# Performance work log

Measured on AMD Instinct MI355X. Metric: run time of the kernel, lower is better.

Reference implementation:

```python
import jax, jax.numpy as jnp
import numpy as np

N = 2_097_152  # number of pose pairs


def _skew(w):
    # w: [N,3] -> [N,3,3] skew-symmetric matrices
    x, y, z = w[..., 0], w[..., 1], w[..., 2]
    O = jnp.zeros_like(x)
    return jnp.stack([
        jnp.stack([O, -z, y], -1),
        jnp.stack([z, O, -x], -1),
        jnp.stack([-y, x, O], -1),
    ], -2)


def _exp_se3(xi):
    # xi: [N,6] twist = [rot_vec(3), trans(3)] -> (R:[N,3,3], t:[N,3])
    w, v = xi[..., :3], xi[..., 3:]
    t2 = jnp.sum(w * w, -1)                      # theta^2
    small = t2 < 1e-8
    t2s = jnp.where(small, 1.0, t2)              # safe denominator
    th = jnp.sqrt(t2s)
    A = jnp.where(small, 1.0 - t2 / 6.0, jnp.sin(th) / th)
    B = jnp.where(small, 0.5 - t2 / 24.0, (1.0 - jnp.cos(th)) / t2s)
    C = jnp.where(small, 1.0 / 6.0 - t2 / 120.0, (th - jnp.sin(th)) / (t2s * th))
    K = _skew(w)
    K2 = K @ K
    I = jnp.eye(3, dtype=xi.dtype)
    R = I + A[..., None, None] * K + B[..., None, None] * K2
    V = I + B[..., None, None] * K + C[..., None, None] * K2
    t = jnp.einsum('nij,nj->ni', V, v)
    return R, t


def _log_se3(R, t):
    # SE(3) log map: (R:[N,3,3], t:[N,3]) -> (w:[N,3], v:[N,3])
    tr = R[..., 0, 0] + R[..., 1, 1] + R[..., 2, 2]
    c = jnp.clip((tr - 1.0) * 0.5, -1.0 + 1e-7, 1.0 - 1e-7)
    th = jnp.arccos(c)
    small = th < 1e-4
    s = jnp.sin(th)
    ths = jnp.where(small, 1.0, th)
    ss = jnp.where(small, 1.0, s)
    coef = jnp.where(small, 0.5 + th * th / 12.0, th / (2.0 * ss))
    wvec = coef[..., None] * jnp.stack([
        R[..., 2, 1] - R[..., 1, 2],
        R[..., 0, 2] - R[..., 2, 0],
        R[..., 1, 0] - R[..., 0, 1],
    ], -1)
    K = _skew(wvec)
    K2 = K @ K
    one_m_c = jnp.where(small, 1.0, 1.0 - c)
    D = jnp.where(small, 1.0 / 12.0,
                  (1.0 - th * s / (2.0 * one_m_c)) / (ths * ths))
    I = jnp.eye(3, dtype=R.dtype)
    Vinv = I - 0.5 * K + D[..., None, None] * K2
    vvec = jnp.einsum('nij,nj->ni', Vinv, t)
    return wvec, vvec


def setup_inputs() -> dict:
    key = jax.random.key(0)
    k1, k2 = jax.random.split(key)
    predict = jax.random.normal(k1, (N, 6), dtype=jnp.float32)
    target = jax.random.normal(k2, (N, 6), dtype=jnp.float32)
    return {"predict": predict, "target": target}


def reference(predict, target):
    # per-sample SE(3) geodesic loss, reduction='mean'
    Rp, tp = _exp_se3(predict)
    Rt, tt = _exp_se3(target)
    # relative transform T_pred^{-1} T_target
    Rd = jnp.einsum('nji,njk->nik', Rp, Rt)           # Rp^T @ Rt
    td = jnp.einsum('nji,nj->ni', Rp, tt - tp)        # Rp^T (tt - tp)
    w, v = _log_se3(Rd, td)
    loss = jnp.sum(w * w, -1) + jnp.sum(v * v, -1)    # squared twist norm [N]
    return jnp.mean(loss)
```

## Files before the change

### kernel.cpp

```cpp
#include <hip/hip_runtime.h>

#define BLOCK 256
#define GRID1 8192

__device__ __forceinline__ float frcp(float x)  { return __builtin_amdgcn_rcpf(x); }
__device__ __forceinline__ float fsqrt_(float x){ return __builtin_amdgcn_sqrtf(x); }

__device__ __forceinline__ float facos(float x) {
    float a = fabsf(x);
    float p = fmaf(a, -0.0187293f, 0.0742610f);
    p = fmaf(a, p, -0.2121144f);
    p = fmaf(a, p, 1.5707288f);
    float r = fsqrt_(1.0f - a) * p;
    return x < 0.0f ? 3.14159265358979f - r : r;
}

__device__ __forceinline__ void expse3(float wx, float wy, float wz,
                                       float vx, float vy, float vz,
                                       float* R, float* t)
{
    float xx = wx*wx, yy = wy*wy, zz = wz*wz;
    float t2 = xx + yy + zz;
    float th = fsqrt_(t2);
    float s, c;
    __sincosf(th, &s, &c);
    float rth = frcp(th);
    float rt2 = rth * rth;
    float A = s * rth;
    float B = (1.0f - c) * rt2;
    float C = (1.0f - A) * rt2;
    float Axz = A*wz, Axy = A*wy, Axx = A*wx;
    float Bxy = B*wx*wy, Bxz = B*wx*wz, Byz = B*wy*wz;
    R[0] = 1.0f + B*(xx - t2); R[1] = Bxy - Axz;          R[2] = Bxz + Axy;
    R[3] = Bxy + Axz;          R[4] = 1.0f + B*(yy - t2); R[5] = Byz - Axx;
    R[6] = Bxz - Axy;          R[7] = Byz + Axx;          R[8] = 1.0f + B*(zz - t2);
    float Bwx = B*wx, Bwy = B*wy, Bwz = B*wz;
    float Cxy = C*wx*wy, Cxz = C*wx*wz, Cyz = C*wy*wz;
    float V0 = 1.0f + C*(xx - t2), V1 = Cxy - Bwz,          V2 = Cxz + Bwy;
    float V3 = Cxy + Bwz,          V4 = 1.0f + C*(yy - t2), V5 = Cyz - Bwx;
    float V6 = Cxz - Bwy,          V7 = Cyz + Bwx,          V8 = 1.0f + C*(zz - t2);
    t[0] = V0*vx + V1*vy + V2*vz;
    t[1] = V3*vx + V4*vy + V5*vz;
    t[2] = V6*vx + V7*vy + V8*vz;
}

__global__ void __launch_bounds__(BLOCK)
se3_loss_stage1(const float* __restrict__ pred, const float* __restrict__ targ,
                float* __restrict__ partial, int n)
{
    int tid = blockIdx.x * BLOCK + threadIdx.x;
    float acc = 0.0f;
    if (tid < n) {
        const float2* p2 = reinterpret_cast<const float2*>(pred) + 3 * (size_t)tid;
        const float2* q2 = reinterpret_cast<const float2*>(targ) + 3 * (size_t)tid;
        float2 pa = p2[0], pb = p2[1], pc = p2[2];
        float2 qa = q2[0], qb = q2[1], qc = q2[2];

        float Rp[9], tp[3], Rt[9], tt[3];
        expse3(pa.x, pa.y, pb.x, pb.y, pc.x, pc.y, Rp, tp);
        expse3(qa.x, qa.y, qb.x, qb.y, qc.x, qc.y, Rt, tt);

        float d0 = tt[0] - tp[0], d1 = tt[1] - tp[1], d2 = tt[2] - tp[2];
        float Rd[9];
        #pragma unroll
        for (int ii = 0; ii < 3; ii++)
            #pragma unroll
            for (int kk = 0; kk < 3; kk++)
                Rd[ii*3+kk] = Rp[0+ii]*Rt[0+kk] + Rp[3+ii]*Rt[3+kk] + Rp[6+ii]*Rt[6+kk];
        float td0 = Rp[0]*d0 + Rp[3]*d1 + Rp[6]*d2;
        float td1 = Rp[1]*d0 + Rp[4]*d1 + Rp[7]*d2;
        float td2 = Rp[2]*d0 + Rp[5]*d1 + Rp[8]*d2;

        float tr = Rd[0] + Rd[4] + Rd[8];
        float c  = fminf(fmaxf((tr - 1.0f) * 0.5f, -1.0f + 1e-7f), 1.0f - 1e-7f);
        float th = facos(c);
        float s  = fsqrt_(fmaxf(1.0f - c*c, 0.0f));
        float coef = th * 0.5f * frcp(s);
        float wx = coef * (Rd[7] - Rd[5]);
        float wy = coef * (Rd[2] - Rd[6]);
        float wz = coef * (Rd[3] - Rd[1]);
        float w2 = fmaf(wx, wx, fmaf(wy, wy, wz * wz));
        float rth = frcp(th);
        float D = (1.0f - th * s * 0.5f * frcp(1.0f - c)) * rth * rth;
        float Dxy = D*wx*wy, Dxz = D*wx*wz, Dyz = D*wy*wz;
        float Vi0 = 1.0f + D*(wx*wx - w2), Vi1 =  0.5f*wz + Dxy,        Vi2 = -0.5f*wy + Dxz;
        float Vi3 = -0.5f*wz + Dxy,        Vi4 = 1.0f + D*(wy*wy - w2), Vi5 =  0.5f*wx + Dyz;
        float Vi6 =  0.5f*wy + Dxz,        Vi7 = -0.5f*wx + Dyz,        Vi8 = 1.0f + D*(wz*wz - w2);
        float vx = Vi0*td0 + Vi1*td1 + Vi2*td2;
        float vy = Vi3*td0 + Vi4*td1 + Vi5*td2;
        float vz = Vi6*td0 + Vi7*td1 + Vi8*td2;

        acc = w2 + fmaf(vx, vx, fmaf(vy, vy, vz * vz));
    }

    #pragma unroll
    for (int off = 32; off; off >>= 1) acc += __shfl_down(acc, off, 64);
    __shared__ float wsum[BLOCK / 64];
    int lane = threadIdx.x & 63, wid = threadIdx.x >> 6;
    if (lane == 0) wsum[wid] = acc;
    __syncthreads();
    if (threadIdx.x == 0) {
        float s = 0.0f;
        #pragma unroll
        for (int k = 0; k < BLOCK / 64; k++) s += wsum[k];
        partial[blockIdx.x] = s;
    }
}

__global__ void __launch_bounds__(BLOCK)
se3_loss_stage2(const float4* __restrict__ partial, float* __restrict__ out,
                float invN)
{
    float acc = 0.0f;
    #pragma unroll
    for (int k = 0; k < GRID1 / 4 / BLOCK; k++) {
        float4 v = partial[threadIdx.x + k * BLOCK];
        acc += (v.x + v.y) + (v.z + v.w);
    }
    #pragma unroll
    for (int off = 32; off; off >>= 1) acc += __shfl_down(acc, off, 64);
    __shared__ float wsum[BLOCK / 64];
    int lane = threadIdx.x & 63, wid = threadIdx.x >> 6;
    if (lane == 0) wsum[wid] = acc;
    __syncthreads();
    if (threadIdx.x == 0) {
        float s = 0.0f;
        #pragma unroll
        for (int k = 0; k < BLOCK / 64; k++) s += wsum[k];
        out[0] = s * invN;
    }
}

extern "C" void kernel_launch(void* const* d_in, const int* in_sizes, int n_in,
                              void* d_out, int out_size, void* d_ws, size_t ws_size,
                              hipStream_t stream) {
    const float* pred = (const float*)d_in[0];
    const float* targ = (const float*)d_in[1];
    float* out = (float*)d_out;
    float* partial = (float*)d_ws;
    int n = in_sizes[0] / 6;
    se3_loss_stage1<<<GRID1, BLOCK, 0, stream>>>(pred, targ, partial, n);
    se3_loss_stage2<<<1, BLOCK, 0, stream>>>((const float4*)partial, out,
                                             1.0f / (float)n);
}
```

Before: 116.0 us.

## Replace rotation matrices with quaternions and cross-product forms in SE3 loss

Rewrites the exp map to produce a unit quaternion via half-angle sincos, and applies V via two cross products instead of a 3x3 matrix. The relative rotation is computed as a quaternion product, the translation rotation uses the quaternion cross-product formula, and the log-map rotation angle and axis come directly from the quaternion. The inverse V matrix is likewise applied with cross products. This cuts the per-thread arithmetic and register use of a compute-heavy kernel, at the cost of slightly different floating-point rounding and angle-clamping behaviour.

```diff
diff --git a/kernel.cpp b/kernel.cpp
--- a/kernel.cpp
+++ b/kernel.cpp
@@ -15,33 +15,29 @@
     return x < 0.0f ? 3.14159265358979f - r : r;
 }
 
-__device__ __forceinline__ void expse3(float wx, float wy, float wz,
-                                       float vx, float vy, float vz,
-                                       float* R, float* t)
+__device__ __forceinline__ void expse3q(float wx, float wy, float wz,
+                                        float vx, float vy, float vz,
+                                        float4* q, float* t)
 {
-    float xx = wx*wx, yy = wy*wy, zz = wz*wz;
-    float t2 = xx + yy + zz;
+    float t2 = fmaf(wx, wx, fmaf(wy, wy, wz * wz));
     float th = fsqrt_(t2);
-    float s, c;
-    __sincosf(th, &s, &c);
+    float sh, ch;
+    __sincosf(0.5f * th, &sh, &ch);
     float rth = frcp(th);
-    float rt2 = rth * rth;
-    float A = s * rth;
-    float B = (1.0f - c) * rt2;
-    float C = (1.0f - A) * rt2;
-    float Axz = A*wz, Axy = A*wy, Axx = A*wx;
-    float Bxy = B*wx*wy, Bxz = B*wx*wz, Byz = B*wy*wz;
-    R[0] = 1.0f + B*(xx - t2); R[1] = Bxy - Axz;          R[2] = Bxz + Axy;
-    R[3] = Bxy + Axz;          R[4] = 1.0f + B*(yy - t2); R[5] = Byz - Axx;
-    R[6] = Bxz - Axy;          R[7] = Byz + Axx;          R[8] = 1.0f + B*(zz - t2);
-    float Bwx = B*wx, Bwy = B*wy, Bwz = B*wz;
-    float Cxy = C*wx*wy, Cxz = C*wx*wz, Cyz = C*wy*wz;
-    float V0 = 1.0f + C*(xx - t2), V1 = Cxy - Bwz,          V2 = Cxz + Bwy;
-    float V3 = Cxy + Bwz,          V4 = 1.0f + C*(yy - t2), V5 = Cyz - Bwx;
-    float V6 = Cxz - Bwy,          V7 = Cyz + Bwx,          V8 = 1.0f + C*(zz - t2);
-    t[0] = V0*vx + V1*vy + V2*vz;
-    t[1] = V3*vx + V4*vy + V5*vz;
-    t[2] = V6*vx + V7*vy + V8*vz;
+    float srt = sh * rth;
+    float A = 2.0f * ch * srt;
+    float B = 2.0f * srt * srt;
+    float C = (1.0f - A) * (rth * rth);
+    q->x = ch; q->y = srt * wx; q->z = srt * wy; q->w = srt * wz;
+    float c1x = fmaf(wy, vz, -wz * vy);
+    float c1y = fmaf(wz, vx, -wx * vz);
+    float c1z = fmaf(wx, vy, -wy * vx);
+    float c2x = fmaf(wy, c1z, -wz * c1y);
+    float c2y = fmaf(wz, c1x, -wx * c1z);
+    float c2z = fmaf(wx, c1y, -wy * c1x);
+    t[0] = fmaf(C, c2x, fmaf(B, c1x, vx));
+    t[1] = fmaf(C, c2y, fmaf(B, c1y, vy));
+    t[2] = fmaf(C, c2z, fmaf(B, c1z, vz));
 }
 
 __global__ void __launch_bounds__(BLOCK)
@@ -56,39 +52,46 @@
         float2 pa = p2[0], pb = p2[1], pc = p2[2];
         float2 qa = q2[0], qb = q2[1], qc = q2[2];
 
-        float Rp[9], tp[3], Rt[9], tt[3];
-        expse3(pa.x, pa.y, pb.x, pb.y, pc.x, pc.y, Rp, tp);
-        expse3(qa.x, qa.y, qb.x, qb.y, qc.x, qc.y, Rt, tt);
+        float4 qp, qt; float tp[3], tt[3];
+        expse3q(pa.x, pa.y, pb.x, pb.y, pc.x, pc.y, &qp, tp);
+        expse3q(qa.x, qa.y, qb.x, qb.y, qc.x, qc.y, &qt, tt);
+
+        float dw = fmaf(qp.x, qt.x, fmaf(qp.y, qt.y, fmaf(qp.z, qt.z, qp.w * qt.w)));
+        float dx = fmaf(qp.x, qt.y, -qp.y * qt.x) - fmaf(qp.z, qt.w, -qp.w * qt.z);
+        float dy = fmaf(qp.x, qt.z, -qp.z * qt.x) - fmaf(qp.w, qt.y, -qp.y * qt.w);
+        float dz = fmaf(qp.x, qt.w, -qp.w * qt.x) - fmaf(qp.y, qt.z, -qp.z * qt.y);
 
         float d0 = tt[0] - tp[0], d1 = tt[1] - tp[1], d2 = tt[2] - tp[2];
-        float Rd[9];
-        #pragma unroll
-        for (int ii = 0; ii < 3; ii++)
-            #pragma unroll
-            for (int kk = 0; kk < 3; kk++)
-                Rd[ii*3+kk] = Rp[0+ii]*Rt[0+kk] + Rp[3+ii]*Rt[3+kk] + Rp[6+ii]*Rt[6+kk];
-        float td0 = Rp[0]*d0 + Rp[3]*d1 + Rp[6]*d2;
-        float td1 = Rp[1]*d0 + Rp[4]*d1 + Rp[7]*d2;
-        float td2 = Rp[2]*d0 + Rp[5]*d1 + Rp[8]*d2;
+        float c1x = fmaf(qp.z, d2, -qp.w * d1);
+        float c1y = fmaf(qp.w, d0, -qp.y * d2);
+        float c1z = fmaf(qp.y, d1, -qp.z * d0);
+        float c2x = fmaf(qp.z, c1z, -qp.w * c1y);
+        float c2y = fmaf(qp.w, c1x, -qp.y * c1z);
+        float c2z = fmaf(qp.y, c1y, -qp.z * c1x);
+        float m2pw = -2.0f * qp.x;
+        float td0 = fmaf(m2pw, c1x, fmaf(2.0f, c2x, d0));
+        float td1 = fmaf(m2pw, c1y, fmaf(2.0f, c2y, d1));
+        float td2 = fmaf(m2pw, c1z, fmaf(2.0f, c2z, d2));
 
-        float tr = Rd[0] + Rd[4] + Rd[8];
-        float c  = fminf(fmaxf((tr - 1.0f) * 0.5f, -1.0f + 1e-7f), 1.0f - 1e-7f);
+        float s2 = fmaf(dx, dx, fmaf(dy, dy, dz * dz));
+        float c  = fminf(fmaxf(fmaf(-2.0f, s2, 1.0f), -1.0f + 1e-7f), 1.0f - 1e-7f);
         float th = facos(c);
-        float s  = fsqrt_(fmaxf(1.0f - c*c, 0.0f));
-        float coef = th * 0.5f * frcp(s);
-        float wx = coef * (Rd[7] - Rd[5]);
-        float wy = coef * (Rd[2] - Rd[6]);
-        float wz = coef * (Rd[3] - Rd[1]);
+        float sn = fsqrt_(fmaxf(fmaf(-c, c, 1.0f), 0.0f));
+        float rsn = frcp(sn);
+        float k  = 2.0f * dw * th * rsn;
+        float wx = k * dx, wy = k * dy, wz = k * dz;
         float w2 = fmaf(wx, wx, fmaf(wy, wy, wz * wz));
         float rth = frcp(th);
-        float D = (1.0f - th * s * 0.5f * frcp(1.0f - c)) * rth * rth;
-        float Dxy = D*wx*wy, Dxz = D*wx*wz, Dyz = D*wy*wz;
-        float Vi0 = 1.0f + D*(wx*wx - w2), Vi1 =  0.5f*wz + Dxy,        Vi2 = -0.5f*wy + Dxz;
-        float Vi3 = -0.5f*wz + Dxy,        Vi4 = 1.0f + D*(wy*wy - w2), Vi5 =  0.5f*wx + Dyz;
-        float Vi6 =  0.5f*wy + Dxz,        Vi7 = -0.5f*wx + Dyz,        Vi8 = 1.0f + D*(wz*wz - w2);
-        float vx = Vi0*td0 + Vi1*td1 + Vi2*td2;
-        float vy = Vi3*td0 + Vi4*td1 + Vi5*td2;
-        float vz = Vi6*td0 + Vi7*td1 + Vi8*td2;
+        float D = (1.0f - th * sn * 0.5f * frcp(1.0f - c)) * (rth * rth);
+        float c3x = fmaf(wy, td2, -wz * td1);
+        float c3y = fmaf(wz, td0, -wx * td2);
+        float c3z = fmaf(wx, td1, -wy * td0);
+        float c4x = fmaf(wy, c3z, -wz * c3y);
+        float c4y = fmaf(wz, c3x, -wx * c3z);
+        float c4z = fmaf(wx, c3y, -wy * c3x);
+        float vx = fmaf(D, c4x, fmaf(-0.5f, c3x, td0));
+        float vy = fmaf(D, c4y, fmaf(-0.5f, c3y, td1));
+        float vz = fmaf(D, c4z, fmaf(-0.5f, c3z, td2));
 
         acc = w2 + fmaf(vx, vx, fmaf(vy, vy, vz * vz));
     }
@@ -102,7 +105,7 @@
     if (threadIdx.x == 0) {
         float s = 0.0f;
         #pragma unroll
-        for (int k = 0; k < BLOCK / 64; k++) s += wsum[k];
+        for (int k2 = 0; k2 < BLOCK / 64; k2++) s += wsum[k2];
         partial[blockIdx.x] = s;
     }
 }
```

Measured after the change: 113.1 us. 1.03x faster.
